# Performance work log

Hardware: AMD Instinct MI355X
Metric: run time of the kernel (lower is better)

## Reference

```python
import jax, jax.numpy as jnp
import numpy as np

# pseudo_image_dims = [512, 512] -> canvas_x = dims[0], canvas_y = dims[1]
CANVAS_X = 512
CANVAS_Y = 512
SHIFT_SIZE = 2          # gen_index_shift(2, ...) -> 5x5 neighborhood
VR_THRESH = 0.1
B = 2
N_LI = 1_000_000
N_RA = 500_000


def setup_inputs() -> dict:
    key = jax.random.key(0)
    k1, k2, k3, k4 = jax.random.split(key, 4)
    li_input = jax.random.normal(k1, (B, N_LI, 4), dtype=jnp.float32)
    ra_input = jax.random.normal(k2, (B, N_RA, 5), dtype=jnp.float32)
    # voxel_coords (y, x) per valid point; batch column is implicitly 0
    li_coords = jax.random.randint(k3, (B, N_LI, 2), 0, CANVAS_Y).astype(jnp.int32)
    ra_coords = jax.random.randint(k4, (B, N_RA, 2), 0, CANVAS_Y).astype(jnp.int32)
    # all points valid; identity point_idxes (deterministic scatter)
    li_point_idxes = jnp.broadcast_to(jnp.arange(N_LI, dtype=jnp.int32), (B, N_LI))
    ra_point_idxes = jnp.broadcast_to(jnp.arange(N_RA, dtype=jnp.int32), (B, N_RA))
    return {
        "li_input": li_input,
        "li_coords": li_coords,
        "li_point_idxes": li_point_idxes,
        "ra_input": ra_input,
        "ra_coords": ra_coords,
        "ra_point_idxes": ra_point_idxes,
    }


def _per_batch(li_pts, li_coor, li_valid, ra_pts, ra_coor, ra_valid):
    X, Y = CANVAS_X, CANVAS_Y
    # flat BEV index per valid point: y * canvas_x + x, scattered to full point set
    li_flat = (li_coor[:, 0] * X + li_coor[:, 1]).astype(jnp.int32)
    li_ind = jnp.zeros(li_pts.shape[0], jnp.int32).at[li_valid].set(li_flat)
    ra_flat = (ra_coor[:, 0] * X + ra_coor[:, 1]).astype(jnp.int32)
    ra_ind = jnp.zeros(ra_pts.shape[0], jnp.int32).at[ra_valid].set(ra_flat)

    vr = jnp.abs(ra_pts[:, 4])
    ra_dy = vr > VR_THRESH

    # DynamicScatter(average_points=False): per-voxel MAX of |vr|; a voxel is
    # dynamic if its max |vr| > 0.1. Empty voxels -> -inf identity -> not dynamic.
    vox_max = jax.ops.segment_max(vr[ra_valid], ra_flat, num_segments=Y * X)
    dyn = (vox_max > VR_THRESH).reshape(Y, X)

    # expand each dynamic voxel to its 5x5 neighborhood with the original's
    # wrap logic: y is modded by (dims[0]+1), x by (dims[1]+1); shifted cells
    # landing on the extra row/col (== dim) are dropped.
    ys = jnp.arange(Y, dtype=jnp.int32)[:, None]   # [Y,1]
    xs = jnp.arange(X, dtype=jnp.int32)[None, :]   # [1,X]
    neigh = jnp.zeros(Y * X, dtype=jnp.int32)
    for i in range(-SHIFT_SIZE, SHIFT_SIZE + 1):
        for j in range(-SHIFT_SIZE, SHIFT_SIZE + 1):
            sy = (ys + i) % (X + 1)   # grid_size[0] = pseudo_image_dims[0] + 1
            sx = (xs + j) % (Y + 1)   # grid_size[1] = pseudo_image_dims[1] + 1
            valid = dyn & (sy < Y) & (sx < X)      # [Y,X]
            flat = sy * X + sx                      # [Y,X]
            flat = jnp.where(valid, flat, 0)
            neigh = neigh.at[flat.reshape(-1)].max(valid.reshape(-1).astype(jnp.int32))
    neigh_mask = neigh > 0          # [Y*X] bool

    li_dy = neigh_mask[li_ind]      # points with matching flat index become dynamic
    return li_dy, li_ind, ra_dy, ra_ind


def reference(li_input, li_coords, li_point_idxes, ra_input, ra_coords, ra_point_idxes):
    return jax.vmap(_per_batch)(li_input, li_coords, li_point_idxes,
                                ra_input, ra_coords, ra_point_idxes)
```

## Files before the change

### kernel.cpp

```cpp
#include <hip/hip_runtime.h>

#define CANVAS 512
#define PLANE (CANVAS * CANVAS)
#define WORDS (PLANE / 32)
#define GRIDW 513
#define BATCH 2
#define N_LI 1000000
#define N_RA 500000

typedef int int2v __attribute__((ext_vector_type(2)));
typedef int int4v __attribute__((ext_vector_type(4)));

__global__ void zero_dyn(uint32_t* __restrict__ p, int nwords) {
    int i = blockIdx.x * blockDim.x + threadIdx.x;
    if (i < nwords) p[i] = 0u;
}

__global__ __launch_bounds__(256) void ra_kernel(
        const float* __restrict__ ra_input,
        const int*   __restrict__ ra_coords,
        int* __restrict__ ra_dy_out,
        int* __restrict__ ra_ind_out,
        unsigned char* __restrict__ dyn) {
    int i = blockIdx.x * blockDim.x + threadIdx.x;
    if (i >= BATCH * N_RA / 2) return;
    int4v c = __builtin_nontemporal_load((const int4v*)ra_coords + i);
    float vr0 = fabsf(__builtin_nontemporal_load(ra_input + (size_t)i * 10 + 4));
    float vr1 = fabsf(__builtin_nontemporal_load(ra_input + (size_t)i * 10 + 9));
    int flat0 = c.x * CANVAS + c.y;
    int flat1 = c.z * CANVAS + c.w;
    int dy0 = vr0 > 0.1f ? 1 : 0;
    int dy1 = vr1 > 0.1f ? 1 : 0;

    int2v dyv;  dyv.x = dy0;   dyv.y = dy1;
    int2v indv; indv.x = flat0; indv.y = flat1;
    __builtin_nontemporal_store(dyv,  (int2v*)ra_dy_out + i);
    __builtin_nontemporal_store(indv, (int2v*)ra_ind_out + i);

    int b = i / (N_RA / 2);
    unsigned char* db = dyn + (size_t)b * PLANE;
    if (dy0) db[flat0] = 1;
    if (dy1) db[flat1] = 1;
}

__global__ __launch_bounds__(256) void dilate_kernel(
        const unsigned char* __restrict__ dyn,
        uint32_t* __restrict__ neighw) {
    int idx  = blockIdx.x * blockDim.x + threadIdx.x;
    int b    = idx >> 18;
    int cell = idx & (PLANE - 1);
    int ty = cell >> 9;
    int tx = cell & (CANVAS - 1);
    const unsigned char* d = dyn + (size_t)b * PLANE;

    int acc = 0;
#pragma unroll
    for (int off = -2; off <= 2; ++off) {
        int sy = ty - off;
        sy += (sy < 0)      ? GRIDW : 0;
        sy -= (sy >= GRIDW) ? GRIDW : 0;
        bool vy = (sy < CANVAS);
        int rowbase = (vy ? sy : 0) * CANVAS;
#pragma unroll
        for (int off2 = -2; off2 <= 2; ++off2) {
            int sx = tx - off2;
            sx += (sx < 0)      ? GRIDW : 0;
            sx -= (sx >= GRIDW) ? GRIDW : 0;
            bool vx = (sx < CANVAS);
            int v = d[rowbase + (vx ? sx : 0)];
            acc |= (vy && vx) ? v : 0;
        }
    }
    unsigned long long m = __ballot(acc != 0);
    int lane = threadIdx.x & 63;
    if (lane == 0)       neighw[idx >> 5] = (uint32_t)m;
    else if (lane == 32) neighw[idx >> 5] = (uint32_t)(m >> 32);
}

__global__ __launch_bounds__(256) void li_kernel(
        const int* __restrict__ li_coords,
        const uint32_t* __restrict__ neighw,
        int* __restrict__ li_dy_out,
        int* __restrict__ li_ind_out) {
    int i = blockIdx.x * blockDim.x + threadIdx.x;
    if (i >= BATCH * N_LI / 2) return;
    int4v c = __builtin_nontemporal_load((const int4v*)li_coords + i);
    int flat0 = c.x * CANVAS + c.y;
    int flat1 = c.z * CANVAS + c.w;
    int b = i / (N_LI / 2);
    const uint32_t* nb = neighw + (size_t)b * WORDS;
    uint32_t w0 = nb[flat0 >> 5];
    uint32_t w1 = nb[flat1 >> 5];
    int2v dyv;
    dyv.x = (int)((w0 >> (flat0 & 31)) & 1u);
    dyv.y = (int)((w1 >> (flat1 & 31)) & 1u);
    int2v indv; indv.x = flat0; indv.y = flat1;
    __builtin_nontemporal_store(indv, (int2v*)li_ind_out + i);
    __builtin_nontemporal_store(dyv,  (int2v*)li_dy_out + i);
}

extern "C" void kernel_launch(void* const* d_in, const int* in_sizes, int n_in,
                              void* d_out, int out_size, void* d_ws, size_t ws_size,
                              hipStream_t stream) {
    const int*   li_coords = (const int*)d_in[1];
    const float* ra_input  = (const float*)d_in[3];
    const int*   ra_coords = (const int*)d_in[4];

    int* out        = (int*)d_out;
    int* li_dy_out  = out;
    int* li_ind_out = out + (size_t)BATCH * N_LI;
    int* ra_dy_out  = out + (size_t)2 * BATCH * N_LI;
    int* ra_ind_out = out + (size_t)2 * BATCH * N_LI + (size_t)BATCH * N_RA;

    unsigned char* dyn    = (unsigned char*)d_ws;
    uint32_t*      neighw = (uint32_t*)(dyn + (size_t)BATCH * PLANE);

    const int nwords = BATCH * PLANE / 4;
    zero_dyn<<<(nwords + 255) / 256, 256, 0, stream>>>((uint32_t*)dyn, nwords);

    const int ra_pairs = BATCH * N_RA / 2;
    ra_kernel<<<(ra_pairs + 255) / 256, 256, 0, stream>>>(
        ra_input, ra_coords, ra_dy_out, ra_ind_out, dyn);

    dilate_kernel<<<BATCH * PLANE / 256, 256, 0, stream>>>(dyn, neighw);

    const int li_pairs = BATCH * N_LI / 2;
    li_kernel<<<(li_pairs + 255) / 256, 256, 0, stream>>>(
        li_coords, neighw, li_dy_out, li_ind_out);
}
```

Baseline: 132.7 us.

## Fuse all stages into one persistent kernel with grid barriers and bitmask dilation

Replaces the four launches (zero, ra scatter, dilate, li lookup) with a single persistent kernel of 1024 blocks that uses atomic-counter grid barriers between phases. The dynamic-voxel map becomes a bit-packed word array set with atomicOr, and dilation runs on 32-bit words using shifts and neighbouring-word carries instead of 25 byte loads per cell. The aim is to remove launch overheads and cut dilation memory traffic. In exchange it adds atomic contention on the bitmap and relies on all 1024 blocks being co-resident, or the spin barrier deadlocks.

```diff
diff --git a/kernel.cpp b/kernel.cpp
--- a/kernel.cpp
+++ b/kernel.cpp
@@ -2,101 +2,104 @@
 
 #define CANVAS 512
 #define PLANE (CANVAS * CANVAS)
-#define WORDS (PLANE / 32)
+#define WORDS_PB 8192
+#define ROWW 16
 #define GRIDW 513
 #define BATCH 2
 #define N_LI 1000000
 #define N_RA 500000
 
+#define NBLK 1024
+#define NTHR 256
+#define TOTTHR (NBLK * NTHR)
+
 typedef int int2v __attribute__((ext_vector_type(2)));
 typedef int int4v __attribute__((ext_vector_type(4)));
 
-__global__ void zero_dyn(uint32_t* __restrict__ p, int nwords) {
-    int i = blockIdx.x * blockDim.x + threadIdx.x;
-    if (i < nwords) p[i] = 0u;
+__device__ __forceinline__ void grid_barrier(unsigned int* cnt) {
+    __syncthreads();
+    if (threadIdx.x == 0) {
+        __hip_atomic_fetch_add(cnt, 1u, __ATOMIC_RELEASE, __HIP_MEMORY_SCOPE_AGENT);
+        while (__hip_atomic_load(cnt, __ATOMIC_RELAXED, __HIP_MEMORY_SCOPE_AGENT) < NBLK)
+            __builtin_amdgcn_s_sleep(2);
+        __builtin_amdgcn_fence(__ATOMIC_ACQUIRE, "agent");
+    }
+    __syncthreads();
 }
 
-__global__ __launch_bounds__(256) void ra_kernel(
+__global__ __launch_bounds__(NTHR, 4) void fused_kernel(
         const float* __restrict__ ra_input,
         const int*   __restrict__ ra_coords,
-        int* __restrict__ ra_dy_out,
-        int* __restrict__ ra_ind_out,
-        unsigned char* __restrict__ dyn) {
-    int i = blockIdx.x * blockDim.x + threadIdx.x;
-    if (i >= BATCH * N_RA / 2) return;
-    int4v c = __builtin_nontemporal_load((const int4v*)ra_coords + i);
-    float vr0 = fabsf(__builtin_nontemporal_load(ra_input + (size_t)i * 10 + 4));
-    float vr1 = fabsf(__builtin_nontemporal_load(ra_input + (size_t)i * 10 + 9));
-    int flat0 = c.x * CANVAS + c.y;
-    int flat1 = c.z * CANVAS + c.w;
-    int dy0 = vr0 > 0.1f ? 1 : 0;
-    int dy1 = vr1 > 0.1f ? 1 : 0;
+        const int*   __restrict__ li_coords,
+        int* __restrict__ li_dy,  int* __restrict__ li_ind,
+        int* __restrict__ ra_dy,  int* __restrict__ ra_ind,
+        unsigned int* __restrict__ dynw,
+        unsigned int* __restrict__ neighw,
+        unsigned int* __restrict__ cnt) {
+    const int tid = blockIdx.x * NTHR + threadIdx.x;
 
-    int2v dyv;  dyv.x = dy0;   dyv.y = dy1;
-    int2v indv; indv.x = flat0; indv.y = flat1;
-    __builtin_nontemporal_store(dyv,  (int2v*)ra_dy_out + i);
-    __builtin_nontemporal_store(indv, (int2v*)ra_ind_out + i);
+    for (int i = tid; i < BATCH * N_RA / 2; i += TOTTHR) {
+        int4v c = __builtin_nontemporal_load((const int4v*)ra_coords + i);
+        float vr0 = fabsf(__builtin_nontemporal_load(ra_input + (size_t)i * 10 + 4));
+        float vr1 = fabsf(__builtin_nontemporal_load(ra_input + (size_t)i * 10 + 9));
+        int flat0 = c.x * CANVAS + c.y;
+        int flat1 = c.z * CANVAS + c.w;
+        int dy0 = vr0 > 0.1f ? 1 : 0;
+        int dy1 = vr1 > 0.1f ? 1 : 0;
+        int2v dyv;  dyv.x = dy0;   dyv.y = dy1;
+        int2v indv; indv.x = flat0; indv.y = flat1;
+        __builtin_nontemporal_store(dyv,  (int2v*)ra_dy  + i);
+        __builtin_nontemporal_store(indv, (int2v*)ra_ind + i);
+        unsigned int* dw = dynw + (i / (N_RA / 2)) * WORDS_PB;
+        if (dy0) atomicOr(&dw[flat0 >> 5], 1u << (flat0 & 31));
+        if (dy1) atomicOr(&dw[flat1 >> 5], 1u << (flat1 & 31));
+    }
+    grid_barrier(&cnt[0]);
 
-    int b = i / (N_RA / 2);
-    unsigned char* db = dyn + (size_t)b * PLANE;
-    if (dy0) db[flat0] = 1;
-    if (dy1) db[flat1] = 1;
-}
+    if (tid < BATCH * WORDS_PB) {
+        int b = tid >> 13;
+        int w = tid & (WORDS_PB - 1);
+        int r = w >> 4;
+        int c = w & (ROWW - 1);
+        const unsigned int* D = dynw + b * WORDS_PB;
+        unsigned int v0 = 0, vm = 0, vp = 0, vfirst = 0, vlast = 0;
+#pragma unroll
+        for (int off = -2; off <= 2; ++off) {
+            int rr = r - off;
+            rr += (rr < 0)      ? GRIDW : 0;
+            rr -= (rr >= GRIDW) ? GRIDW : 0;
+            if (rr < CANVAS) {
+                const unsigned int* R = D + rr * ROWW;
+                v0 |= R[c];
+                vm |= (c > 0)        ? R[c - 1] : 0u;
+                vp |= (c < ROWW - 1) ? R[c + 1] : 0u;
+                vfirst |= R[0];
+                vlast  |= R[ROWW - 1];
+            }
+        }
+        unsigned int out = v0 | (v0 << 1) | (v0 << 2) | (v0 >> 1) | (v0 >> 2)
+                         | (vm >> 30) | (vm >> 31)
+                         | (vp << 31) | (vp << 30);
+        if (c == 0)        out |= (vlast >> 31);
+        if (c == ROWW - 1) out |= (vfirst << 31);
+        neighw[tid] = out;
+    }
+    grid_barrier(&cnt[1]);
 
-__global__ __launch_bounds__(256) void dilate_kernel(
-        const unsigned char* __restrict__ dyn,
-        uint32_t* __restrict__ neighw) {
-    int idx  = blockIdx.x * blockDim.x + threadIdx.x;
-    int b    = idx >> 18;
-    int cell = idx & (PLANE - 1);
-    int ty = cell >> 9;
-    int tx = cell & (CANVAS - 1);
-    const unsigned char* d = dyn + (size_t)b * PLANE;
-
-    int acc = 0;
-#pragma unroll
-    for (int off = -2; off <= 2; ++off) {
-        int sy = ty - off;
-        sy += (sy < 0)      ? GRIDW : 0;
-        sy -= (sy >= GRIDW) ? GRIDW : 0;
-        bool vy = (sy < CANVAS);
-        int rowbase = (vy ? sy : 0) * CANVAS;
-#pragma unroll
-        for (int off2 = -2; off2 <= 2; ++off2) {
-            int sx = tx - off2;
-            sx += (sx < 0)      ? GRIDW : 0;
-            sx -= (sx >= GRIDW) ? GRIDW : 0;
-            bool vx = (sx < CANVAS);
-            int v = d[rowbase + (vx ? sx : 0)];
-            acc |= (vy && vx) ? v : 0;
-        }
+    for (int i = tid; i < BATCH * N_LI / 2; i += TOTTHR) {
+        int4v c = __builtin_nontemporal_load((const int4v*)li_coords + i);
+        int flat0 = c.x * CANVAS + c.y;
+        int flat1 = c.z * CANVAS + c.w;
+        const unsigned int* nb = neighw + (i / (N_LI / 2)) * WORDS_PB;
+        unsigned int w0 = nb[flat0 >> 5];
+        unsigned int w1 = nb[flat1 >> 5];
+        int2v dyv;
+        dyv.x = (int)((w0 >> (flat0 & 31)) & 1u);
+        dyv.y = (int)((w1 >> (flat1 & 31)) & 1u);
+        int2v indv; indv.x = flat0; indv.y = flat1;
+        __builtin_nontemporal_store(indv, (int2v*)li_ind + i);
+        __builtin_nontemporal_store(dyv,  (int2v*)li_dy  + i);
     }
-    unsigned long long m = __ballot(acc != 0);
-    int lane = threadIdx.x & 63;
-    if (lane == 0)       neighw[idx >> 5] = (uint32_t)m;
-    else if (lane == 32) neighw[idx >> 5] = (uint32_t)(m >> 32);
-}
-
-__global__ __launch_bounds__(256) void li_kernel(
-        const int* __restrict__ li_coords,
-        const uint32_t* __restrict__ neighw,
-        int* __restrict__ li_dy_out,
-        int* __restrict__ li_ind_out) {
-    int i = blockIdx.x * blockDim.x + threadIdx.x;
-    if (i >= BATCH * N_LI / 2) return;
-    int4v c = __builtin_nontemporal_load((const int4v*)li_coords + i);
-    int flat0 = c.x * CANVAS + c.y;
-    int flat1 = c.z * CANVAS + c.w;
-    int b = i / (N_LI / 2);
-    const uint32_t* nb = neighw + (size_t)b * WORDS;
-    uint32_t w0 = nb[flat0 >> 5];
-    uint32_t w1 = nb[flat1 >> 5];
-    int2v dyv;
-    dyv.x = (int)((w0 >> (flat0 & 31)) & 1u);
-    dyv.y = (int)((w1 >> (flat1 & 31)) & 1u);
-    int2v indv; indv.x = flat0; indv.y = flat1;
-    __builtin_nontemporal_store(indv, (int2v*)li_ind_out + i);
-    __builtin_nontemporal_store(dyv,  (int2v*)li_dy_out + i);
 }
 
 extern "C" void kernel_launch(void* const* d_in, const int* in_sizes, int n_in,
@@ -112,19 +115,14 @@
     int* ra_dy_out  = out + (size_t)2 * BATCH * N_LI;
     int* ra_ind_out = out + (size_t)2 * BATCH * N_LI + (size_t)BATCH * N_RA;
 
-    unsigned char* dyn    = (unsigned char*)d_ws;
-    uint32_t*      neighw = (uint32_t*)(dyn + (size_t)BATCH * PLANE);
+    unsigned int* neighw = (unsigned int*)d_ws;
+    unsigned int* dynw   = neighw + (size_t)BATCH * WORDS_PB;
+    unsigned int* cnt    = dynw   + (size_t)BATCH * WORDS_PB;
 
-    const int nwords = BATCH * PLANE / 4;
-    zero_dyn<<<(nwords + 255) / 256, 256, 0, stream>>>((uint32_t*)dyn, nwords);
+    hipMemsetAsync(dynw, 0, (size_t)BATCH * WORDS_PB * 4 + 64, stream);
 
-    const int ra_pairs = BATCH * N_RA / 2;
-    ra_kernel<<<(ra_pairs + 255) / 256, 256, 0, stream>>>(
-        ra_input, ra_coords, ra_dy_out, ra_ind_out, dyn);
-
-    dilate_kernel<<<BATCH * PLANE / 256, 256, 0, stream>>>(dyn, neighw);
-
-    const int li_pairs = BATCH * N_LI / 2;
-    li_kernel<<<(li_pairs + 255) / 256, 256, 0, stream>>>(
-        li_coords, neighw, li_dy_out, li_ind_out);
+    fused_kernel<<<NBLK, NTHR, 0, stream>>>(
+        ra_input, ra_coords, li_coords,
+        li_dy_out, li_ind_out, ra_dy_out, ra_ind_out,
+        dynw, neighw, cnt);
 }
```

Measured after the change: 313.4 us. 136% more time.
